# Kernel optimization log

Hardware: AMD Instinct MI355X
Metric: run time of the kernel (lower is better)

Reference implementation:

```python
import jax, jax.numpy as jnp
import numpy as np

B, O, L, E = 8, 4, 1024, 1024
BETA = 512
NSEG = 12
OUT = 1


def setup_inputs() -> dict:
    key = jax.random.key(0)
    ks = jax.random.split(key, 8)
    hidden = jax.random.normal(ks[0], (B, O, L, E), jnp.float32)
    # strictly increasing boundaries in (1, L), shared across the O options (as in the torch code)
    raw = jnp.sort(jax.random.randint(ks[1], (B, NSEG), 2, L - NSEG), axis=-1)
    idx = raw + jnp.arange(NSEG, dtype=raw.dtype)
    s = 0.02
    Wp = jax.random.normal(ks[2], (E, 2 * BETA), jnp.float32) * s
    bp = jnp.zeros((2 * BETA,), jnp.float32)
    Wa0 = jax.random.normal(ks[3], (2 * BETA, BETA), jnp.float32) * s
    ba0 = jnp.zeros((BETA,), jnp.float32)
    Wa = jax.random.normal(ks[4], (BETA, BETA), jnp.float32) * s
    ba = jnp.zeros((BETA,), jnp.float32)
    Wl0 = jax.random.normal(ks[5], (8 * BETA, BETA), jnp.float32) * s
    bl0 = jnp.zeros((BETA,), jnp.float32)
    Wl = jax.random.normal(ks[6], (BETA, OUT), jnp.float32) * s
    bl = jnp.zeros((OUT,), jnp.float32)
    return dict(hidden=hidden, idx=idx, Wp=Wp, bp=bp, Wa0=Wa0, ba0=ba0,
                Wa=Wa, ba=ba, Wl0=Wl0, bl0=bl0, Wl=Wl, bl=bl)


def _seg_mean(P, starts, ends):
    # P: [B,O,L+1,E] exclusive prefix sums; starts/ends: [B,K] token offsets.
    s = jnp.take_along_axis(P, starts[:, None, :, None], axis=2)
    e = jnp.take_along_axis(P, ends[:, None, :, None], axis=2)
    cnt = (ends - starts).astype(P.dtype)[:, None, :, None]
    return (e - s) / cnt  # [B,O,K,E]


def _get_param(x, Wp, bp):
    e = 1.0 + jax.nn.relu(x @ Wp + bp)
    a, b = jnp.split(e, 2, axis=-1)
    return a, b


def _attn_pool(a, b, Wa0, ba0, Wa, ba):
    # attention-weighted reduction over axis -2 (the 'logic' operator)
    h = jax.nn.relu(jnp.concatenate([a, b], axis=-1) @ Wa0 + ba0)
    w = jax.nn.softmax(h @ Wa + ba, axis=-2)
    return (w * a).sum(axis=-2), (w * b).sum(axis=-2)


def reference(hidden, idx, Wp, bp, Wa0, ba0, Wa, ba, Wl0, bl0, Wl, bl):
    # ---- init_embed: ragged segment means via prefix sums (one pass, no host syncs)
    P = jnp.concatenate([jnp.zeros_like(hidden[:, :, :1]),
                         jnp.cumsum(hidden, axis=2)], axis=2)  # [B,O,L+1,E]
    ones = jnp.ones((idx.shape[0], 1), idx.dtype)
    starts_c = jnp.concatenate([ones, idx[:, :NSEG - 3]], axis=1)  # [B, NSEG-2]
    ends_c = idx[:, :NSEG - 2]
    ctx = _seg_mean(P, starts_c, ends_c)                                # [B,O,Nc,E]
    q = _seg_mean(P, idx[:, NSEG - 3:NSEG - 2], idx[:, NSEG - 2:NSEG - 1])[:, :, 0]
    o = _seg_mean(P, idx[:, NSEG - 2:NSEG - 1], idx[:, NSEG - 1:NSEG])[:, :, 0]
    allc = _seg_mean(P, ones, idx[:, NSEG - 3:NSEG - 2])[:, :, 0]       # [B,O,E]
    # ---- beta params for context segments
    a_c, b_c = _get_param(ctx, Wp, bp)                                  # [B,O,Nc,BETA]
    # intersection over segments
    ia, ib = _attn_pool(a_c, b_c, Wa0, ba0, Wa, ba)                     # [B,O,BETA]
    # renew: pair each segment with the intersection, pool over the pair axis
    pa = jnp.stack([a_c, jnp.broadcast_to(ia[:, :, None, :], a_c.shape)], axis=-2)
    pb = jnp.stack([b_c, jnp.broadcast_to(ib[:, :, None, :], b_c.shape)], axis=-2)
    na, nb = _attn_pool(pa, pb, Wa0, ba0, Wa, ba)                       # [B,O,Nc,BETA]
    # union: invert, attention-pool over segments, invert back
    ua, ub = _attn_pool(1.0 / na, 1.0 / nb, Wa0, ba0, Wa, ba)
    ua, ub = 1.0 / ua, 1.0 / ub                                         # [B,O,BETA]
    # ---- beta params for question / option / whole-context spans
    a_q, b_q = _get_param(q, Wp, bp)
    a_o, b_o = _get_param(o, Wp, bp)
    a_ac, b_ac = _get_param(allc, Wp, bp)
    # ---- classify head: concat 4 beta embeddings -> 8*BETA -> MLP -> logits
    cat = jnp.concatenate([ua, ub, a_ac, b_ac, a_o, b_o, a_q, b_q], axis=-1)
    h = jax.nn.relu(cat @ Wl0 + bl0)
    return h @ Wl + bl  # [B,O,OUT]
```

## Files before the change

kernel.cpp:

```cpp
#include <hip/hip_runtime.h>
#include <hip/hip_bf16.h>

#define B_    8
#define O_    4
#define L_    1024
#define E_    1024
#define BETA_ 512
#define NSEG_ 12
#define BO_   32
#define NCH_  16

enum : size_t {
  WS_SPART = 0,
  WS_X     = WS_SPART + (size_t)BO_ * NCH_ * 12 * E_,
  WS_P1P   = WS_X     + (size_t)BO_ * 13 * E_,
  WS_H1P   = WS_P1P   + (size_t)8  * BO_ * 13 * E_,
  WS_T1P   = WS_H1P   + (size_t)16 * BO_ * 10 * BETA_,
  WS_H2P   = WS_T1P   + (size_t)8  * BO_ * 10 * BETA_,
  WS_T2P   = WS_H2P   + (size_t)8  * BO_ * BETA_,
  WS_H3P   = WS_T2P   + (size_t)8  * BO_ * BETA_,
  WS_T3P   = WS_H3P   + (size_t)16 * BO_ * 10 * BETA_,
  WS_HFP   = WS_T3P   + (size_t)8  * BO_ * 10 * BETA_,
  WS_TE    = WS_HFP   + (size_t)32 * BO_ * BETA_,
  WS_T1B   = WS_TE    + (size_t)BO_ * 13 * E_,
  WS_IAB   = WS_T1B   + (size_t)BO_ * 10 * BETA_,
  WS_RN    = WS_IAB   + (size_t)BO_ * 2 * BETA_,
  WS_END   = WS_RN    + (size_t)BO_ * 10 * E_,
};

__device__ __forceinline__ float relu_(float v) { return v > 0.f ? v : 0.f; }

__global__ void k1_segsum(const float* __restrict__ hidden, const int* __restrict__ idx,
                          float* __restrict__ Spart) {
    const int chunk = blockIdx.x;
    const int bo = blockIdx.y;
    const int b = bo >> 2;
    int cuts[13];
    cuts[0] = 1;
#pragma unroll
    for (int i = 0; i < 12; ++i) cuts[i + 1] = idx[b * NSEG_ + i];
    const int e4 = threadIdx.x << 2;
    float* sp = Spart + ((size_t)(bo * NCH_ + chunk) * 12) * E_ + e4;
    const float4 z = make_float4(0.f, 0.f, 0.f, 0.f);
#pragma unroll
    for (int m = 0; m < 12; ++m) *reinterpret_cast<float4*>(sp + (size_t)m * E_) = z;
    const int l0 = chunk * 64;
    const int l1 = l0 + 64;
    int lo = l0 < 1 ? 1 : l0;
    const int hi = l1 < cuts[12] ? l1 : cuts[12];
    if (lo >= hi) return;
    const float* base = hidden + (size_t)bo * (L_ * E_) + e4;
    int j = 0;
    while (j < 11 && cuts[j + 1] <= lo) ++j;
    int l = lo;
    while (l < hi) {
        const int e2 = (j < 11 && cuts[j + 1] < hi) ? cuts[j + 1] : hi;
        float sx = 0.f, sy = 0.f, sz = 0.f, sw = 0.f;
        for (; l < e2; ++l) {
            const float4 v = *reinterpret_cast<const float4*>(base + (size_t)l * E_);
            sx += v.x; sy += v.y; sz += v.z; sw += v.w;
        }
        float4 s; s.x = sx; s.y = sy; s.z = sz; s.w = sw;
        *reinterpret_cast<float4*>(sp + (size_t)j * E_) = s;
        ++j;
    }
}

__global__ __launch_bounds__(256) void k2_means(
    const float* __restrict__ Spart, const int* __restrict__ idx,
    float* __restrict__ X) {
    const int bo = blockIdx.y;
    const int col = blockIdx.x * 256 + threadIdx.x;
    const int b = bo >> 2;
    int cuts[13];
    cuts[0] = 1;
#pragma unroll
    for (int i = 0; i < 12; ++i) cuts[i + 1] = idx[b * NSEG_ + i];
    const float* sp = Spart + (size_t)bo * NCH_ * 12 * E_ + col;
    float allc = 0.f;
#pragma unroll
    for (int m = 0; m < 12; ++m) {
        float s = 0.f;
#pragma unroll
        for (int ch = 0; ch < NCH_; ++ch) s += sp[((size_t)ch * 12 + m) * E_];
        X[((size_t)bo * 13 + m) * E_ + col] = s / (float)(cuts[m + 1] - cuts[m]);
        if (m < 10) allc += s;
    }
    X[((size_t)bo * 13 + 12) * E_ + col] = allc / (float)(cuts[10] - 1);
}

template<int M, int ML, int K, int N, int KC, int BOG, int XF, int NPART>
__global__ __launch_bounds__(256) void gemm_sk(
    const float* __restrict__ Xb, const float* __restrict__ xbias,
    const float* __restrict__ W, float* __restrict__ OUT,
    const float* __restrict__ A0, const float* __restrict__ A1,
    const float* __restrict__ A2, const float* __restrict__ A3,
    float* __restrict__ SIDE, float* __restrict__ SIDE2) {
    const int kidx = blockIdx.x;
    const int k0 = kidx * KC;
    const int bo0 = blockIdx.y * BOG;
    const int c = blockIdx.z * 256 + threadIdx.x;
    const int tid = threadIdx.x;
    __shared__ __align__(16) float xs[BOG * ML * KC];

    for (int i = tid; i < BOG * ML * KC; i += 256) {
        const int kk = i % KC;
        const int rm = i / KC;
        const int m = rm % ML;
        const int bb = rm / ML;
        const int bo = bo0 + bb;
        const int k = k0 + kk;
        float v;
        if constexpr (XF == 0) {
            v = Xb[((size_t)bo * ML + m) * K + k];
        } else if constexpr (XF == 1) {
            float s = xbias[k];
#pragma unroll
            for (int p = 0; p < NPART; ++p)
                s += Xb[(((size_t)p * BO_ + bo) * ML + m) * K + k];
            v = 1.f + relu_(s);
            SIDE[((size_t)bo * ML + m) * K + k] = v;
        } else if constexpr (XF == 2) {
            float s = xbias[k];
#pragma unroll
            for (int p = 0; p < NPART; ++p)
                s += Xb[(((size_t)p * BO_ + bo) * ML + m) * K + k];
            v = relu_(s);
        } else if constexpr (XF == 4) {
            const int col = k & 511, half = k >> 9;
            const float bac = A2[col];
            float t[10], mx = -1e30f;
#pragma unroll
            for (int j = 0; j < 10; ++j) {
                float s = bac;
#pragma unroll
                for (int p = 0; p < NPART; ++p)
                    s += A0[(((size_t)p * BO_ + bo) * 10 + j) * BETA_ + col];
                t[j] = s;
                mx = fmaxf(mx, s);
            }
            if (half == 0) {
#pragma unroll
                for (int j = 0; j < 10; ++j)
                    SIDE2[((size_t)bo * 10 + j) * BETA_ + col] = t[j];
            }
            float sw = 0.f, acc = 0.f;
#pragma unroll
            for (int j = 0; j < 10; ++j) {
                const float pj = expf(t[j] - mx);
                sw += pj;
                acc = fmaf(pj, A1[((size_t)bo * 13 + j) * E_ + half * BETA_ + col], acc);
            }
            v = acc / sw;
            SIDE[(size_t)bo * 1024 + k] = v;
        } else if constexpr (XF == 5) {
            const int col = k & 511, half = k >> 9;
            const float tj = A0[((size_t)bo * 10 + m) * BETA_ + col];
            float tI = A2[col];
#pragma unroll
            for (int p = 0; p < NPART; ++p)
                tI += A1[((size_t)p * BO_ + bo) * BETA_ + col];
            const float mx = fmaxf(tj, tI);
            const float e0 = expf(tj - mx);
            const float e1 = expf(tI - mx);
            const float ea = A3[((size_t)bo * 13 + m) * E_ + half * BETA_ + col];
            const float iv = SIDE2[(size_t)bo * 1024 + k];
            v = (e0 + e1) / (e0 * ea + e1 * iv);
            SIDE[((size_t)bo * 10 + m) * E_ + k] = v;
        } else {
            if (k < 1024) {
                const int col = k & 511, half = k >> 9;
                const float bac = A2[col];
                float t[10], mx = -1e30f;
#pragma unroll
                for (int j = 0; j < 10; ++j) {
                    float s = bac;
#pragma unroll
                    for (int p = 0; p < NPART; ++p)
                        s += A0[(((size_t)p * BO_ + bo) * 10 + j) * BETA_ + col];
                    t[j] = s;
                    mx = fmaxf(mx, s);
                }
                float sw = 0.f, acc = 0.f;
#pragma unroll
                for (int j = 0; j < 10; ++j) {
                    const float pj = expf(t[j] - mx);
                    sw += pj;
                    acc = fmaf(pj, A1[((size_t)bo * 10 + j) * E_ + k], acc);
                }
                v = sw / acc;
            } else {
                const int region = k >> 10;
                const int row = (region == 1) ? 12 : (region == 2) ? 11 : 10;
                v = A3[((size_t)bo * 13 + row) * E_ + (k & 1023)];
            }
        }
        xs[i] = v;
    }
    __syncthreads();

    float acc[BOG][M];
#pragma unroll
    for (int b = 0; b < BOG; ++b)
#pragma unroll
        for (int m = 0; m < M; ++m) acc[b][m] = 0.f;
    const float* __restrict__ wp = W + (size_t)k0 * N + c;
    for (int k4 = 0; k4 < KC / 4; ++k4) {
        const float w0 = wp[(size_t)(4 * k4 + 0) * N];
        const float w1 = wp[(size_t)(4 * k4 + 1) * N];
        const float w2 = wp[(size_t)(4 * k4 + 2) * N];
        const float w3 = wp[(size_t)(4 * k4 + 3) * N];
#pragma unroll
        for (int b = 0; b < BOG; ++b) {
#pragma unroll
            for (int m = 0; m < M; ++m) {
                const float4 xv = *reinterpret_cast<const float4*>(&xs[(b * ML + m) * KC + 4 * k4]);
                float a = acc[b][m];
                a = fmaf(xv.x, w0, a);
                a = fmaf(xv.y, w1, a);
                a = fmaf(xv.z, w2, a);
                a = fmaf(xv.w, w3, a);
                acc[b][m] = a;
            }
        }
    }
#pragma unroll
    for (int b = 0; b < BOG; ++b) {
        float* op = OUT + (((size_t)kidx * BO_ + bo0 + b) * M) * N + c;
#pragma unroll
        for (int m = 0; m < M; ++m) op[(size_t)m * N] = acc[b][m];
    }
}

__global__ void __launch_bounds__(512) k_final(
    const float* __restrict__ HFP, const float* __restrict__ bl0,
    const float* __restrict__ Wl, const float* __restrict__ bl,
    float* __restrict__ out) {
    const int bo = blockIdx.x;
    const int c = threadIdx.x;
    float s = bl0[c];
#pragma unroll
    for (int p = 0; p < 32; ++p) s += HFP[((size_t)p * BO_ + bo) * BETA_ + c];
    float partial = relu_(s) * Wl[c];
#pragma unroll
    for (int off = 32; off > 0; off >>= 1) partial += __shfl_down(partial, off, 64);
    __shared__ float red[8];
    if ((c & 63) == 0) red[c >> 6] = partial;
    __syncthreads();
    if (c == 0) out[bo] = red[0] + red[1] + red[2] + red[3] + red[4] + red[5] + red[6] + red[7] + bl[0];
}

extern "C" void kernel_launch(void* const* d_in, const int* in_sizes, int n_in,
                              void* d_out, int out_size, void* d_ws, size_t ws_size,
                              hipStream_t stream) {
    const float* hidden = (const float*)d_in[0];
    const int* idx = (const int*)d_in[1];
    const float* Wp  = (const float*)d_in[2];
    const float* bp  = (const float*)d_in[3];
    const float* Wa0 = (const float*)d_in[4];
    const float* ba0 = (const float*)d_in[5];
    const float* Wa  = (const float*)d_in[6];
    const float* ba  = (const float*)d_in[7];
    const float* Wl0 = (const float*)d_in[8];
    const float* bl0 = (const float*)d_in[9];
    const float* Wl  = (const float*)d_in[10];
    const float* bl  = (const float*)d_in[11];
    float* ws = (float*)d_ws;
    float* SPART = ws + WS_SPART;
    float* X     = ws + WS_X;
    float* P1P   = ws + WS_P1P;
    float* H1P   = ws + WS_H1P;
    float* T1P   = ws + WS_T1P;
    float* H2P   = ws + WS_H2P;
    float* T2P   = ws + WS_T2P;
    float* H3P   = ws + WS_H3P;
    float* T3P   = ws + WS_T3P;
    float* HFP   = ws + WS_HFP;
    float* TE    = ws + WS_TE;
    float* T1B   = ws + WS_T1B;
    float* IAB   = ws + WS_IAB;
    float* RN    = ws + WS_RN;
    const float* NUL = nullptr;

    k1_segsum<<<dim3(NCH_, BO_), 256, 0, stream>>>(hidden, idx, SPART);
    k2_means<<<dim3(4, BO_), 256, 0, stream>>>(SPART, idx, X);
    gemm_sk<13, 13, 1024, 1024, 128, 2, 0, 1>
        <<<dim3(8, 16, 4), 256, 0, stream>>>(X, NUL, Wp, P1P, NUL, NUL, NUL, NUL, nullptr, nullptr);
    gemm_sk<10, 13, 1024, 512, 64, 2, 1, 8>
        <<<dim3(16, 16, 2), 256, 0, stream>>>(P1P, bp, Wa0, H1P, NUL, NUL, NUL, NUL, TE, nullptr);
    gemm_sk<10, 10, 512, 512, 64, 2, 2, 16>
        <<<dim3(8, 16, 2), 256, 0, stream>>>(H1P, ba0, Wa, T1P, NUL, NUL, NUL, NUL, nullptr, nullptr);
    gemm_sk<1, 1, 1024, 512, 128, 8, 4, 8>
        <<<dim3(8, 4, 2), 256, 0, stream>>>(NUL, NUL, Wa0, H2P, T1P, TE, ba, NUL, IAB, T1B);
    gemm_sk<1, 1, 512, 512, 64, 8, 2, 8>
        <<<dim3(8, 4, 2), 256, 0, stream>>>(H2P, ba0, Wa, T2P, NUL, NUL, NUL, NUL, nullptr, nullptr);
    gemm_sk<10, 10, 1024, 512, 64, 2, 5, 8>
        <<<dim3(16, 16, 2), 256, 0, stream>>>(NUL, NUL, Wa0, H3P, T1B, T2P, ba, TE, RN, IAB);
    gemm_sk<10, 10, 512, 512, 64, 2, 2, 16>
        <<<dim3(8, 16, 2), 256, 0, stream>>>(H3P, ba0, Wa, T3P, NUL, NUL, NUL, NUL, nullptr, nullptr);
    gemm_sk<1, 1, 4096, 512, 128, 8, 6, 8>
        <<<dim3(32, 4, 2), 256, 0, stream>>>(NUL, NUL, Wl0, HFP, T3P, RN, ba, TE, nullptr, nullptr);
    k_final<<<BO_, 512, 0, stream>>>(HFP, bl0, Wl, bl, (float*)d_out);
}
```

Before: 164.9 us.

## Unfuse GEMM prologues into separate reduction kernels and double segment-sum chunking

The split-K partial reductions, activations and softmax pooling that each GEMM used to compute in its shared-memory prologue move into small standalone kernels (t_te, t_hrelu, t_iab, t_rn, t_cat). The GEMM becomes a plain kernel that reads its input rows straight from global memory with float4 loads and has no shared staging. This removes the redundant prologue work repeated across every N-block, at the cost of more kernel launches and extra workspace round trips. The segment-sum pass also uses 32 chunks of 32 tokens instead of 16 of 64 and stops zero-filling partials; the means kernel now sums only the chunks that overlap each segment.

```diff
diff --git a/kernel.cpp b/kernel.cpp
--- a/kernel.cpp
+++ b/kernel.cpp
@@ -8,24 +8,28 @@
 #define BETA_ 512
 #define NSEG_ 12
 #define BO_   32
-#define NCH_  16
+#define NCH_  32
 
 enum : size_t {
   WS_SPART = 0,
   WS_X     = WS_SPART + (size_t)BO_ * NCH_ * 12 * E_,
   WS_P1P   = WS_X     + (size_t)BO_ * 13 * E_,
-  WS_H1P   = WS_P1P   + (size_t)8  * BO_ * 13 * E_,
-  WS_T1P   = WS_H1P   + (size_t)16 * BO_ * 10 * BETA_,
-  WS_H2P   = WS_T1P   + (size_t)8  * BO_ * 10 * BETA_,
-  WS_T2P   = WS_H2P   + (size_t)8  * BO_ * BETA_,
-  WS_H3P   = WS_T2P   + (size_t)8  * BO_ * BETA_,
-  WS_T3P   = WS_H3P   + (size_t)16 * BO_ * 10 * BETA_,
-  WS_HFP   = WS_T3P   + (size_t)8  * BO_ * 10 * BETA_,
-  WS_TE    = WS_HFP   + (size_t)32 * BO_ * BETA_,
-  WS_T1B   = WS_TE    + (size_t)BO_ * 13 * E_,
+  WS_TE    = WS_P1P   + (size_t)8  * BO_ * 13 * E_,
+  WS_H1P   = WS_TE    + (size_t)BO_ * 13 * E_,
+  WS_H1R   = WS_H1P   + (size_t)16 * BO_ * 10 * BETA_,
+  WS_T1P   = WS_H1R   + (size_t)BO_ * 10 * BETA_,
+  WS_T1B   = WS_T1P   + (size_t)8  * BO_ * 10 * BETA_,
   WS_IAB   = WS_T1B   + (size_t)BO_ * 10 * BETA_,
-  WS_RN    = WS_IAB   + (size_t)BO_ * 2 * BETA_,
-  WS_END   = WS_RN    + (size_t)BO_ * 10 * E_,
+  WS_H2P   = WS_IAB   + (size_t)BO_ * 2 * BETA_,
+  WS_H2R   = WS_H2P   + (size_t)8  * BO_ * BETA_,
+  WS_T2P   = WS_H2R   + (size_t)BO_ * BETA_,
+  WS_RN    = WS_T2P   + (size_t)8  * BO_ * BETA_,
+  WS_H3P   = WS_RN    + (size_t)BO_ * 10 * E_,
+  WS_H3R   = WS_H3P   + (size_t)16 * BO_ * 10 * BETA_,
+  WS_T3P   = WS_H3R   + (size_t)BO_ * 10 * BETA_,
+  WS_CAT   = WS_T3P   + (size_t)8  * BO_ * 10 * BETA_,
+  WS_HFP   = WS_CAT   + (size_t)BO_ * 8 * BETA_,
+  WS_END   = WS_HFP   + (size_t)32 * BO_ * BETA_,
 };
 
 __device__ __forceinline__ float relu_(float v) { return v > 0.f ? v : 0.f; }
@@ -39,17 +43,14 @@
     cuts[0] = 1;
 #pragma unroll
     for (int i = 0; i < 12; ++i) cuts[i + 1] = idx[b * NSEG_ + i];
-    const int e4 = threadIdx.x << 2;
-    float* sp = Spart + ((size_t)(bo * NCH_ + chunk) * 12) * E_ + e4;
-    const float4 z = make_float4(0.f, 0.f, 0.f, 0.f);
-#pragma unroll
-    for (int m = 0; m < 12; ++m) *reinterpret_cast<float4*>(sp + (size_t)m * E_) = z;
-    const int l0 = chunk * 64;
-    const int l1 = l0 + 64;
+    const int l0 = chunk * 32;
+    const int l1 = l0 + 32;
     int lo = l0 < 1 ? 1 : l0;
     const int hi = l1 < cuts[12] ? l1 : cuts[12];
     if (lo >= hi) return;
+    const int e4 = threadIdx.x << 2;
     const float* base = hidden + (size_t)bo * (L_ * E_) + e4;
+    float* sp = Spart + (size_t)(bo * NCH_ + chunk) * 12 * E_ + e4;
     int j = 0;
     while (j < 11 && cuts[j + 1] <= lo) ++j;
     int l = lo;
@@ -80,125 +81,24 @@
     float allc = 0.f;
 #pragma unroll
     for (int m = 0; m < 12; ++m) {
+        const int c0 = cuts[m] >> 5;
+        const int c1 = (cuts[m + 1] - 1) >> 5;
         float s = 0.f;
-#pragma unroll
-        for (int ch = 0; ch < NCH_; ++ch) s += sp[((size_t)ch * 12 + m) * E_];
+        for (int ch = c0; ch <= c1; ++ch) s += sp[((size_t)ch * 12 + m) * E_];
         X[((size_t)bo * 13 + m) * E_ + col] = s / (float)(cuts[m + 1] - cuts[m]);
         if (m < 10) allc += s;
     }
     X[((size_t)bo * 13 + 12) * E_ + col] = allc / (float)(cuts[10] - 1);
 }
 
-template<int M, int ML, int K, int N, int KC, int BOG, int XF, int NPART>
-__global__ __launch_bounds__(256) void gemm_sk(
-    const float* __restrict__ Xb, const float* __restrict__ xbias,
-    const float* __restrict__ W, float* __restrict__ OUT,
-    const float* __restrict__ A0, const float* __restrict__ A1,
-    const float* __restrict__ A2, const float* __restrict__ A3,
-    float* __restrict__ SIDE, float* __restrict__ SIDE2) {
+template<int M, int XM, int K, int N, int KC, int BOG>
+__global__ __launch_bounds__(256) void gemm_u(
+    const float* __restrict__ XR, const float* __restrict__ W,
+    float* __restrict__ OUTP) {
     const int kidx = blockIdx.x;
     const int k0 = kidx * KC;
     const int bo0 = blockIdx.y * BOG;
     const int c = blockIdx.z * 256 + threadIdx.x;
-    const int tid = threadIdx.x;
-    __shared__ __align__(16) float xs[BOG * ML * KC];
-
-    for (int i = tid; i < BOG * ML * KC; i += 256) {
-        const int kk = i % KC;
-        const int rm = i / KC;
-        const int m = rm % ML;
-        const int bb = rm / ML;
-        const int bo = bo0 + bb;
-        const int k = k0 + kk;
-        float v;
-        if constexpr (XF == 0) {
-            v = Xb[((size_t)bo * ML + m) * K + k];
-        } else if constexpr (XF == 1) {
-            float s = xbias[k];
-#pragma unroll
-            for (int p = 0; p < NPART; ++p)
-                s += Xb[(((size_t)p * BO_ + bo) * ML + m) * K + k];
-            v = 1.f + relu_(s);
-            SIDE[((size_t)bo * ML + m) * K + k] = v;
-        } else if constexpr (XF == 2) {
-            float s = xbias[k];
-#pragma unroll
-            for (int p = 0; p < NPART; ++p)
-                s += Xb[(((size_t)p * BO_ + bo) * ML + m) * K + k];
-            v = relu_(s);
-        } else if constexpr (XF == 4) {
-            const int col = k & 511, half = k >> 9;
-            const float bac = A2[col];
-            float t[10], mx = -1e30f;
-#pragma unroll
-            for (int j = 0; j < 10; ++j) {
-                float s = bac;
-#pragma unroll
-                for (int p = 0; p < NPART; ++p)
-                    s += A0[(((size_t)p * BO_ + bo) * 10 + j) * BETA_ + col];
-                t[j] = s;
-                mx = fmaxf(mx, s);
-            }
-            if (half == 0) {
-#pragma unroll
-                for (int j = 0; j < 10; ++j)
-                    SIDE2[((size_t)bo * 10 + j) * BETA_ + col] = t[j];
-            }
-            float sw = 0.f, acc = 0.f;
-#pragma unroll
-            for (int j = 0; j < 10; ++j) {
-                const float pj = expf(t[j] - mx);
-                sw += pj;
-                acc = fmaf(pj, A1[((size_t)bo * 13 + j) * E_ + half * BETA_ + col], acc);
-            }
-            v = acc / sw;
-            SIDE[(size_t)bo * 1024 + k] = v;
-        } else if constexpr (XF == 5) {
-            const int col = k & 511, half = k >> 9;
-            const float tj = A0[((size_t)bo * 10 + m) * BETA_ + col];
-            float tI = A2[col];
-#pragma unroll
-            for (int p = 0; p < NPART; ++p)
-                tI += A1[((size_t)p * BO_ + bo) * BETA_ + col];
-            const float mx = fmaxf(tj, tI);
-            const float e0 = expf(tj - mx);
-            const float e1 = expf(tI - mx);
-            const float ea = A3[((size_t)bo * 13 + m) * E_ + half * BETA_ + col];
-            const float iv = SIDE2[(size_t)bo * 1024 + k];
-            v = (e0 + e1) / (e0 * ea + e1 * iv);
-            SIDE[((size_t)bo * 10 + m) * E_ + k] = v;
-        } else {
-            if (k < 1024) {
-                const int col = k & 511, half = k >> 9;
-                const float bac = A2[col];
-                float t[10], mx = -1e30f;
-#pragma unroll
-                for (int j = 0; j < 10; ++j) {
-                    float s = bac;
-#pragma unroll
-                    for (int p = 0; p < NPART; ++p)
-                        s += A0[(((size_t)p * BO_ + bo) * 10 + j) * BETA_ + col];
-                    t[j] = s;
-                    mx = fmaxf(mx, s);
-                }
-                float sw = 0.f, acc = 0.f;
-#pragma unroll
-                for (int j = 0; j < 10; ++j) {
-                    const float pj = expf(t[j] - mx);
-                    sw += pj;
-                    acc = fmaf(pj, A1[((size_t)bo * 10 + j) * E_ + k], acc);
-                }
-                v = sw / acc;
-            } else {
-                const int region = k >> 10;
-                const int row = (region == 1) ? 12 : (region == 2) ? 11 : 10;
-                v = A3[((size_t)bo * 13 + row) * E_ + (k & 1023)];
-            }
-        }
-        xs[i] = v;
-    }
-    __syncthreads();
-
     float acc[BOG][M];
 #pragma unroll
     for (int b = 0; b < BOG; ++b)
@@ -214,7 +114,8 @@
         for (int b = 0; b < BOG; ++b) {
 #pragma unroll
             for (int m = 0; m < M; ++m) {
-                const float4 xv = *reinterpret_cast<const float4*>(&xs[(b * ML + m) * KC + 4 * k4]);
+                const float4 xv = *reinterpret_cast<const float4*>(
+                    XR + ((size_t)(bo0 + b) * XM + m) * K + k0 + 4 * k4);
                 float a = acc[b][m];
                 a = fmaf(xv.x, w0, a);
                 a = fmaf(xv.y, w1, a);
@@ -226,10 +127,120 @@
     }
 #pragma unroll
     for (int b = 0; b < BOG; ++b) {
-        float* op = OUT + (((size_t)kidx * BO_ + bo0 + b) * M) * N + c;
+        float* op = OUTP + (((size_t)kidx * BO_ + bo0 + b) * M) * N + c;
 #pragma unroll
         for (int m = 0; m < M; ++m) op[(size_t)m * N] = acc[b][m];
     }
+}
+
+__global__ __launch_bounds__(256) void t_te(
+    const float* __restrict__ P1P, const float* __restrict__ bp,
+    float* __restrict__ TE, float* __restrict__ CAT) {
+    const int bo = blockIdx.y;
+    const int i = blockIdx.x * 256 + threadIdx.x;
+    const int m = i >> 10, col = i & 1023;
+    float s = bp[col];
+#pragma unroll
+    for (int p = 0; p < 8; ++p)
+        s += P1P[(((size_t)p * BO_ + bo) * 13 + m) * E_ + col];
+    const float v = 1.f + relu_(s);
+    TE[((size_t)bo * 13 + m) * E_ + col] = v;
+    if (m >= 10) CAT[(size_t)bo * 4096 + (size_t)(13 - m) * 1024 + col] = v;
+}
+
+template<int NPART, int ROWS>
+__global__ __launch_bounds__(256) void t_hrelu(
+    const float* __restrict__ HP, const float* __restrict__ b,
+    float* __restrict__ HR) {
+    const int bo = blockIdx.y;
+    const int i = blockIdx.x * 256 + threadIdx.x;
+    const int col = i & 511;
+    float s = b[col];
+#pragma unroll
+    for (int p = 0; p < NPART; ++p)
+        s += HP[((size_t)p * BO_ + bo) * (ROWS * BETA_) + i];
+    HR[(size_t)bo * (ROWS * BETA_) + i] = relu_(s);
+}
+
+__global__ void __launch_bounds__(512) t_iab(
+    const float* __restrict__ T1P, const float* __restrict__ ba,
+    const float* __restrict__ TE, float* __restrict__ T1B,
+    float* __restrict__ IAB) {
+    const int bo = blockIdx.x;
+    const int c = threadIdx.x;
+    const float bac = ba[c];
+    float t[10], mx = -1e30f;
+#pragma unroll
+    for (int j = 0; j < 10; ++j) {
+        float s = bac;
+#pragma unroll
+        for (int p = 0; p < 8; ++p)
+            s += T1P[(((size_t)p * BO_ + bo) * 10 + j) * BETA_ + c];
+        t[j] = s;
+        T1B[((size_t)bo * 10 + j) * BETA_ + c] = s;
+        mx = fmaxf(mx, s);
+    }
+    float p[10], sw = 0.f;
+#pragma unroll
+    for (int j = 0; j < 10; ++j) { p[j] = expf(t[j] - mx); sw += p[j]; }
+    const float inv = 1.0f / sw;
+    float ia = 0.f, ib = 0.f;
+#pragma unroll
+    for (int j = 0; j < 10; ++j) {
+        const float pj = p[j] * inv;
+        ia = fmaf(pj, TE[((size_t)bo * 13 + j) * E_ + c], ia);
+        ib = fmaf(pj, TE[((size_t)bo * 13 + j) * E_ + BETA_ + c], ib);
+    }
+    IAB[(size_t)bo * 1024 + c] = ia;
+    IAB[(size_t)bo * 1024 + BETA_ + c] = ib;
+}
+
+__global__ __launch_bounds__(256) void t_rn(
+    const float* __restrict__ T1B, const float* __restrict__ T2P,
+    const float* __restrict__ ba, const float* __restrict__ TE,
+    const float* __restrict__ IAB, float* __restrict__ RN) {
+    const int bo = blockIdx.y;
+    const int i = blockIdx.x * 256 + threadIdx.x;
+    const int j = i >> 10, k = i & 1023;
+    const int col = k & 511;
+    const float tj = T1B[((size_t)bo * 10 + j) * BETA_ + col];
+    float tI = ba[col];
+#pragma unroll
+    for (int p = 0; p < 8; ++p)
+        tI += T2P[((size_t)p * BO_ + bo) * BETA_ + col];
+    const float mx = fmaxf(tj, tI);
+    const float e0 = expf(tj - mx);
+    const float e1 = expf(tI - mx);
+    const float ea = TE[((size_t)bo * 13 + j) * E_ + k];
+    const float iv = IAB[(size_t)bo * 1024 + k];
+    RN[((size_t)bo * 10 + j) * E_ + k] = (e0 + e1) / (e0 * ea + e1 * iv);
+}
+
+__global__ __launch_bounds__(256) void t_cat(
+    const float* __restrict__ T3P, const float* __restrict__ ba,
+    const float* __restrict__ RN, float* __restrict__ CAT) {
+    const int bo = blockIdx.y;
+    const int k = blockIdx.x * 256 + threadIdx.x;
+    const int col = k & 511;
+    const float bac = ba[col];
+    float t[10], mx = -1e30f;
+#pragma unroll
+    for (int j = 0; j < 10; ++j) {
+        float s = bac;
+#pragma unroll
+        for (int p = 0; p < 8; ++p)
+            s += T3P[(((size_t)p * BO_ + bo) * 10 + j) * BETA_ + col];
+        t[j] = s;
+        mx = fmaxf(mx, s);
+    }
+    float sw = 0.f, acc = 0.f;
+#pragma unroll
+    for (int j = 0; j < 10; ++j) {
+        const float pj = expf(t[j] - mx);
+        sw += pj;
+        acc = fmaf(pj, RN[((size_t)bo * 10 + j) * E_ + k], acc);
+    }
+    CAT[(size_t)bo * 4096 + k] = sw / acc;
 }
 
 __global__ void __launch_bounds__(512) k_final(
@@ -269,36 +280,46 @@
     float* SPART = ws + WS_SPART;
     float* X     = ws + WS_X;
     float* P1P   = ws + WS_P1P;
+    float* TE    = ws + WS_TE;
     float* H1P   = ws + WS_H1P;
+    float* H1R   = ws + WS_H1R;
     float* T1P   = ws + WS_T1P;
-    float* H2P   = ws + WS_H2P;
-    float* T2P   = ws + WS_T2P;
-    float* H3P   = ws + WS_H3P;
-    float* T3P   = ws + WS_T3P;
-    float* HFP   = ws + WS_HFP;
-    float* TE    = ws + WS_TE;
     float* T1B   = ws + WS_T1B;
     float* IAB   = ws + WS_IAB;
+    float* H2P   = ws + WS_H2P;
+    float* H2R   = ws + WS_H2R;
+    float* T2P   = ws + WS_T2P;
     float* RN    = ws + WS_RN;
-    const float* NUL = nullptr;
+    float* H3P   = ws + WS_H3P;
+    float* H3R   = ws + WS_H3R;
+    float* T3P   = ws + WS_T3P;
+    float* CAT   = ws + WS_CAT;
+    float* HFP   = ws + WS_HFP;
 
     k1_segsum<<<dim3(NCH_, BO_), 256, 0, stream>>>(hidden, idx, SPART);
     k2_means<<<dim3(4, BO_), 256, 0, stream>>>(SPART, idx, X);
-    gemm_sk<13, 13, 1024, 1024, 128, 2, 0, 1>
-        <<<dim3(8, 16, 4), 256, 0, stream>>>(X, NUL, Wp, P1P, NUL, NUL, NUL, NUL, nullptr, nullptr);
-    gemm_sk<10, 13, 1024, 512, 64, 2, 1, 8>
-        <<<dim3(16, 16, 2), 256, 0, stream>>>(P1P, bp, Wa0, H1P, NUL, NUL, NUL, NUL, TE, nullptr);
-    gemm_sk<10, 10, 512, 512, 64, 2, 2, 16>
-        <<<dim3(8, 16, 2), 256, 0, stream>>>(H1P, ba0, Wa, T1P, NUL, NUL, NUL, NUL, nullptr, nullptr);
-    gemm_sk<1, 1, 1024, 512, 128, 8, 4, 8>
-        <<<dim3(8, 4, 2), 256, 0, stream>>>(NUL, NUL, Wa0, H2P, T1P, TE, ba, NUL, IAB, T1B);
-    gemm_sk<1, 1, 512, 512, 64, 8, 2, 8>
-        <<<dim3(8, 4, 2), 256, 0, stream>>>(H2P, ba0, Wa, T2P, NUL, NUL, NUL, NUL, nullptr, nullptr);
-    gemm_sk<10, 10, 1024, 512, 64, 2, 5, 8>
-        <<<dim3(16, 16, 2), 256, 0, stream>>>(NUL, NUL, Wa0, H3P, T1B, T2P, ba, TE, RN, IAB);
-    gemm_sk<10, 10, 512, 512, 64, 2, 2, 16>
-        <<<dim3(8, 16, 2), 256, 0, stream>>>(H3P, ba0, Wa, T3P, NUL, NUL, NUL, NUL, nullptr, nullptr);
-    gemm_sk<1, 1, 4096, 512, 128, 8, 6, 8>
-        <<<dim3(32, 4, 2), 256, 0, stream>>>(NUL, NUL, Wl0, HFP, T3P, RN, ba, TE, nullptr, nullptr);
+    gemm_u<13, 13, 1024, 1024, 128, 2>
+        <<<dim3(8, 16, 4), 256, 0, stream>>>(X, Wp, P1P);
+    t_te<<<dim3(52, BO_), 256, 0, stream>>>(P1P, bp, TE, CAT);
+    gemm_u<10, 13, 1024, 512, 64, 2>
+        <<<dim3(16, 16, 2), 256, 0, stream>>>(TE, Wa0, H1P);
+    t_hrelu<16, 10><<<dim3(20, BO_), 256, 0, stream>>>(H1P, ba0, H1R);
+    gemm_u<10, 10, 512, 512, 64, 2>
+        <<<dim3(8, 16, 2), 256, 0, stream>>>(H1R, Wa, T1P);
+    t_iab<<<BO_, 512, 0, stream>>>(T1P, ba, TE, T1B, IAB);
+    gemm_u<1, 1, 1024, 512, 128, 2>
+        <<<dim3(8, 16, 2), 256, 0, stream>>>(IAB, Wa0, H2P);
+    t_hrelu<8, 1><<<dim3(2, BO_), 256, 0, stream>>>(H2P, ba0, H2R);
+    gemm_u<1, 1, 512, 512, 64, 2>
+        <<<dim3(8, 16, 2), 256, 0, stream>>>(H2R, Wa, T2P);
+    t_rn<<<dim3(40, BO_), 256, 0, stream>>>(T1B, T2P, ba, TE, IAB, RN);
+    gemm_u<10, 10, 1024, 512, 64, 2>
+        <<<dim3(16, 16, 2), 256, 0, stream>>>(RN, Wa0, H3P);
+    t_hrelu<16, 10><<<dim3(20, BO_), 256, 0, stream>>>(H3P, ba0, H3R);
+    gemm_u<10, 10, 512, 512, 64, 2>
+        <<<dim3(8, 16, 2), 256, 0, stream>>>(H3R, Wa, T3P);
+    t_cat<<<dim3(4, BO_), 256, 0, stream>>>(T3P, ba, RN, CAT);
+    gemm_u<1, 1, 4096, 512, 128, 8>
+        <<<dim3(32, 4, 2), 256, 0, stream>>>(CAT, Wl0, HFP);
     k_final<<<BO_, 512, 0, stream>>>(HFP, bl0, Wl, bl, (float*)d_out);
 }
```

Result: slower. 170.8 us (+3.6%).

## Fuse all stages into one cooperative persistent kernel with grid barriers

Applied to the files above, without the earlier changes.

Replaces the eleven separate kernel launches with a single cooperatively launched persistent kernel of 512 blocks. The stages are separated by atomic-counter grid barriers, and each stage loops over its tasks inside the kernel. The segment-sum chunks are halved to 32 rows, and the means stage now reads only the chunks that overlap each segment instead of all of them. Unused chunk partials are no longer zero-filled. The intent is to remove launch and inter-kernel gaps. In exchange it relies on all blocks being co-resident, and spinning barriers cost time on phases that have few tasks.

```diff
diff --git a/kernel.cpp b/kernel.cpp
--- a/kernel.cpp
+++ b/kernel.cpp
@@ -8,167 +8,85 @@
 #define BETA_ 512
 #define NSEG_ 12
 #define BO_   32
-#define NCH_  16
+#define NCH_  32
+#define NBLK  512
 
 enum : size_t {
-  WS_SPART = 0,
+  WS_BAR   = 0,
+  WS_SPART = 64,
   WS_X     = WS_SPART + (size_t)BO_ * NCH_ * 12 * E_,
   WS_P1P   = WS_X     + (size_t)BO_ * 13 * E_,
-  WS_H1P   = WS_P1P   + (size_t)8  * BO_ * 13 * E_,
+  WS_TE    = WS_P1P   + (size_t)8  * BO_ * 13 * E_,
+  WS_H1P   = WS_TE    + (size_t)BO_ * 13 * E_,
   WS_T1P   = WS_H1P   + (size_t)16 * BO_ * 10 * BETA_,
-  WS_H2P   = WS_T1P   + (size_t)8  * BO_ * 10 * BETA_,
+  WS_T1B   = WS_T1P   + (size_t)8  * BO_ * 10 * BETA_,
+  WS_IAB   = WS_T1B   + (size_t)BO_ * 10 * BETA_,
+  WS_H2P   = WS_IAB   + (size_t)BO_ * 2 * BETA_,
   WS_T2P   = WS_H2P   + (size_t)8  * BO_ * BETA_,
-  WS_H3P   = WS_T2P   + (size_t)8  * BO_ * BETA_,
+  WS_RN    = WS_T2P   + (size_t)8  * BO_ * BETA_,
+  WS_H3P   = WS_RN    + (size_t)BO_ * 10 * E_,
   WS_T3P   = WS_H3P   + (size_t)16 * BO_ * 10 * BETA_,
   WS_HFP   = WS_T3P   + (size_t)8  * BO_ * 10 * BETA_,
-  WS_TE    = WS_HFP   + (size_t)32 * BO_ * BETA_,
-  WS_T1B   = WS_TE    + (size_t)BO_ * 13 * E_,
-  WS_IAB   = WS_T1B   + (size_t)BO_ * 10 * BETA_,
-  WS_RN    = WS_IAB   + (size_t)BO_ * 2 * BETA_,
-  WS_END   = WS_RN    + (size_t)BO_ * 10 * E_,
+  WS_END   = WS_HFP   + (size_t)32 * BO_ * BETA_,
 };
 
 __device__ __forceinline__ float relu_(float v) { return v > 0.f ? v : 0.f; }
 
-__global__ void k1_segsum(const float* __restrict__ hidden, const int* __restrict__ idx,
-                          float* __restrict__ Spart) {
-    const int chunk = blockIdx.x;
-    const int bo = blockIdx.y;
-    const int b = bo >> 2;
-    int cuts[13];
-    cuts[0] = 1;
-#pragma unroll
-    for (int i = 0; i < 12; ++i) cuts[i + 1] = idx[b * NSEG_ + i];
-    const int e4 = threadIdx.x << 2;
-    float* sp = Spart + ((size_t)(bo * NCH_ + chunk) * 12) * E_ + e4;
-    const float4 z = make_float4(0.f, 0.f, 0.f, 0.f);
-#pragma unroll
-    for (int m = 0; m < 12; ++m) *reinterpret_cast<float4*>(sp + (size_t)m * E_) = z;
-    const int l0 = chunk * 64;
-    const int l1 = l0 + 64;
-    int lo = l0 < 1 ? 1 : l0;
-    const int hi = l1 < cuts[12] ? l1 : cuts[12];
-    if (lo >= hi) return;
-    const float* base = hidden + (size_t)bo * (L_ * E_) + e4;
-    int j = 0;
-    while (j < 11 && cuts[j + 1] <= lo) ++j;
-    int l = lo;
-    while (l < hi) {
-        const int e2 = (j < 11 && cuts[j + 1] < hi) ? cuts[j + 1] : hi;
-        float sx = 0.f, sy = 0.f, sz = 0.f, sw = 0.f;
-        for (; l < e2; ++l) {
-            const float4 v = *reinterpret_cast<const float4*>(base + (size_t)l * E_);
-            sx += v.x; sy += v.y; sz += v.z; sw += v.w;
-        }
-        float4 s; s.x = sx; s.y = sy; s.z = sz; s.w = sw;
-        *reinterpret_cast<float4*>(sp + (size_t)j * E_) = s;
-        ++j;
-    }
+__device__ __forceinline__ void gbar(unsigned* bar, unsigned tgt, int tid) {
+    __syncthreads();
+    if (tid == 0) {
+        __threadfence();
+        __hip_atomic_fetch_add(bar, 1u, __ATOMIC_RELAXED, __HIP_MEMORY_SCOPE_AGENT);
+        while (__hip_atomic_load(bar, __ATOMIC_RELAXED, __HIP_MEMORY_SCOPE_AGENT) < tgt)
+            __builtin_amdgcn_s_sleep(16);
+        __threadfence();
+    }
+    __syncthreads();
 }
 
-__global__ __launch_bounds__(256) void k2_means(
-    const float* __restrict__ Spart, const int* __restrict__ idx,
-    float* __restrict__ X) {
-    const int bo = blockIdx.y;
-    const int col = blockIdx.x * 256 + threadIdx.x;
-    const int b = bo >> 2;
-    int cuts[13];
-    cuts[0] = 1;
-#pragma unroll
-    for (int i = 0; i < 12; ++i) cuts[i + 1] = idx[b * NSEG_ + i];
-    const float* sp = Spart + (size_t)bo * NCH_ * 12 * E_ + col;
-    float allc = 0.f;
-#pragma unroll
-    for (int m = 0; m < 12; ++m) {
-        float s = 0.f;
-#pragma unroll
-        for (int ch = 0; ch < NCH_; ++ch) s += sp[((size_t)ch * 12 + m) * E_];
-        X[((size_t)bo * 13 + m) * E_ + col] = s / (float)(cuts[m + 1] - cuts[m]);
-        if (m < 10) allc += s;
-    }
-    X[((size_t)bo * 13 + 12) * E_ + col] = allc / (float)(cuts[10] - 1);
-}
-
 template<int M, int ML, int K, int N, int KC, int BOG, int XF, int NPART>
-__global__ __launch_bounds__(256) void gemm_sk(
+__device__ void gemm_phase(
+    const int gid, const int tid, const int NT, float* xs,
     const float* __restrict__ Xb, const float* __restrict__ xbias,
     const float* __restrict__ W, float* __restrict__ OUT,
     const float* __restrict__ A0, const float* __restrict__ A1,
     const float* __restrict__ A2, const float* __restrict__ A3,
     float* __restrict__ SIDE, float* __restrict__ SIDE2) {
-    const int kidx = blockIdx.x;
-    const int k0 = kidx * KC;
-    const int bo0 = blockIdx.y * BOG;
-    const int c = blockIdx.z * 256 + threadIdx.x;
-    const int tid = threadIdx.x;
-    __shared__ __align__(16) float xs[BOG * ML * KC];
-
-    for (int i = tid; i < BOG * ML * KC; i += 256) {
-        const int kk = i % KC;
-        const int rm = i / KC;
-        const int m = rm % ML;
-        const int bb = rm / ML;
-        const int bo = bo0 + bb;
-        const int k = k0 + kk;
-        float v;
-        if constexpr (XF == 0) {
-            v = Xb[((size_t)bo * ML + m) * K + k];
-        } else if constexpr (XF == 1) {
-            float s = xbias[k];
-#pragma unroll
-            for (int p = 0; p < NPART; ++p)
-                s += Xb[(((size_t)p * BO_ + bo) * ML + m) * K + k];
-            v = 1.f + relu_(s);
-            SIDE[((size_t)bo * ML + m) * K + k] = v;
-        } else if constexpr (XF == 2) {
-            float s = xbias[k];
-#pragma unroll
-            for (int p = 0; p < NPART; ++p)
-                s += Xb[(((size_t)p * BO_ + bo) * ML + m) * K + k];
-            v = relu_(s);
-        } else if constexpr (XF == 4) {
-            const int col = k & 511, half = k >> 9;
-            const float bac = A2[col];
-            float t[10], mx = -1e30f;
-#pragma unroll
-            for (int j = 0; j < 10; ++j) {
-                float s = bac;
+    constexpr int NCH = N / 256;
+    constexpr int NBOG = BO_ / BOG;
+    for (int task = gid; task < NT; task += NBLK) {
+        const int nidx = task % NCH;
+        const int rest = task / NCH;
+        const int bidx = rest % NBOG;
+        const int kidx = rest / NBOG;
+        const int k0 = kidx * KC;
+        const int bo0 = bidx * BOG;
+        const int c = nidx * 256 + tid;
+
+        for (int i = tid; i < BOG * ML * KC; i += 256) {
+            const int kk = i % KC;
+            const int rm = i / KC;
+            const int m = rm % ML;
+            const int bb = rm / ML;
+            const int bo = bo0 + bb;
+            const int k = k0 + kk;
+            float v;
+            if constexpr (XF == 0) {
+                v = Xb[((size_t)bo * ML + m) * K + k];
+            } else if constexpr (XF == 1) {
+                float s = xbias[k];
 #pragma unroll
                 for (int p = 0; p < NPART; ++p)
-                    s += A0[(((size_t)p * BO_ + bo) * 10 + j) * BETA_ + col];
-                t[j] = s;
-                mx = fmaxf(mx, s);
-            }
-            if (half == 0) {
-#pragma unroll
-                for (int j = 0; j < 10; ++j)
-                    SIDE2[((size_t)bo * 10 + j) * BETA_ + col] = t[j];
-            }
-            float sw = 0.f, acc = 0.f;
-#pragma unroll
-            for (int j = 0; j < 10; ++j) {
-                const float pj = expf(t[j] - mx);
-                sw += pj;
-                acc = fmaf(pj, A1[((size_t)bo * 13 + j) * E_ + half * BETA_ + col], acc);
-            }
-            v = acc / sw;
-            SIDE[(size_t)bo * 1024 + k] = v;
-        } else if constexpr (XF == 5) {
-            const int col = k & 511, half = k >> 9;
-            const float tj = A0[((size_t)bo * 10 + m) * BETA_ + col];
-            float tI = A2[col];
-#pragma unroll
-            for (int p = 0; p < NPART; ++p)
-                tI += A1[((size_t)p * BO_ + bo) * BETA_ + col];
-            const float mx = fmaxf(tj, tI);
-            const float e0 = expf(tj - mx);
-            const float e1 = expf(tI - mx);
-            const float ea = A3[((size_t)bo * 13 + m) * E_ + half * BETA_ + col];
-            const float iv = SIDE2[(size_t)bo * 1024 + k];
-            v = (e0 + e1) / (e0 * ea + e1 * iv);
-            SIDE[((size_t)bo * 10 + m) * E_ + k] = v;
-        } else {
-            if (k < 1024) {
+                    s += Xb[(((size_t)p * BO_ + bo) * ML + m) * K + k];
+                v = 1.f + relu_(s);
+                SIDE[((size_t)bo * ML + m) * K + k] = v;
+            } else if constexpr (XF == 2) {
+                float s = xbias[k];
+#pragma unroll
+                for (int p = 0; p < NPART; ++p)
+                    s += Xb[(((size_t)p * BO_ + bo) * ML + m) * K + k];
+                v = relu_(s);
+            } else if constexpr (XF == 4) {
                 const int col = k & 511, half = k >> 9;
                 const float bac = A2[col];
                 float t[10], mx = -1e30f;
@@ -181,73 +99,230 @@
                     t[j] = s;
                     mx = fmaxf(mx, s);
                 }
+                if (half == 0) {
+#pragma unroll
+                    for (int j = 0; j < 10; ++j)
+                        SIDE2[((size_t)bo * 10 + j) * BETA_ + col] = t[j];
+                }
                 float sw = 0.f, acc = 0.f;
 #pragma unroll
                 for (int j = 0; j < 10; ++j) {
                     const float pj = expf(t[j] - mx);
                     sw += pj;
-                    acc = fmaf(pj, A1[((size_t)bo * 10 + j) * E_ + k], acc);
-                }
-                v = sw / acc;
+                    acc = fmaf(pj, A1[((size_t)bo * 13 + j) * E_ + half * BETA_ + col], acc);
+                }
+                v = acc / sw;
+                SIDE[(size_t)bo * 1024 + k] = v;
+            } else if constexpr (XF == 5) {
+                const int col = k & 511, half = k >> 9;
+                const float tj = A0[((size_t)bo * 10 + m) * BETA_ + col];
+                float tI = A2[col];
+#pragma unroll
+                for (int p = 0; p < NPART; ++p)
+                    tI += A1[((size_t)p * BO_ + bo) * BETA_ + col];
+                const float mx = fmaxf(tj, tI);
+                const float e0 = expf(tj - mx);
+                const float e1 = expf(tI - mx);
+                const float ea = A3[((size_t)bo * 13 + m) * E_ + half * BETA_ + col];
+                const float iv = SIDE2[(size_t)bo * 1024 + k];
+                v = (e0 + e1) / (e0 * ea + e1 * iv);
+                SIDE[((size_t)bo * 10 + m) * E_ + k] = v;
             } else {
-                const int region = k >> 10;
-                const int row = (region == 1) ? 12 : (region == 2) ? 11 : 10;
-                v = A3[((size_t)bo * 13 + row) * E_ + (k & 1023)];
+                if (k < 1024) {
+                    const int col = k & 511;
+                    const float bac = A2[col];
+                    float t[10], mx = -1e30f;
+#pragma unroll
+                    for (int j = 0; j < 10; ++j) {
+                        float s = bac;
+#pragma unroll
+                        for (int p = 0; p < NPART; ++p)
+                            s += A0[(((size_t)p * BO_ + bo) * 10 + j) * BETA_ + col];
+                        t[j] = s;
+                        mx = fmaxf(mx, s);
+                    }
+                    float sw = 0.f, acc = 0.f;
+#pragma unroll
+                    for (int j = 0; j < 10; ++j) {
+                        const float pj = expf(t[j] - mx);
+                        sw += pj;
+                        acc = fmaf(pj, A1[((size_t)bo * 10 + j) * E_ + k], acc);
+                    }
+                    v = sw / acc;
+                } else {
+                    const int region = k >> 10;
+                    const int row = (region == 1) ? 12 : (region == 2) ? 11 : 10;
+                    v = A3[((size_t)bo * 13 + row) * E_ + (k & 1023)];
+                }
             }
-        }
-        xs[i] = v;
-    }
-    __syncthreads();
-
-    float acc[BOG][M];
-#pragma unroll
-    for (int b = 0; b < BOG; ++b)
-#pragma unroll
-        for (int m = 0; m < M; ++m) acc[b][m] = 0.f;
-    const float* __restrict__ wp = W + (size_t)k0 * N + c;
-    for (int k4 = 0; k4 < KC / 4; ++k4) {
-        const float w0 = wp[(size_t)(4 * k4 + 0) * N];
-        const float w1 = wp[(size_t)(4 * k4 + 1) * N];
-        const float w2 = wp[(size_t)(4 * k4 + 2) * N];
-        const float w3 = wp[(size_t)(4 * k4 + 3) * N];
+            xs[i] = v;
+        }
+        __syncthreads();
+
+        float acc[BOG][M];
+#pragma unroll
+        for (int b = 0; b < BOG; ++b)
+#pragma unroll
+            for (int m = 0; m < M; ++m) acc[b][m] = 0.f;
+        const float* __restrict__ wp = W + (size_t)k0 * N + c;
+        for (int k4 = 0; k4 < KC / 4; ++k4) {
+            const float w0 = wp[(size_t)(4 * k4 + 0) * N];
+            const float w1 = wp[(size_t)(4 * k4 + 1) * N];
+            const float w2 = wp[(size_t)(4 * k4 + 2) * N];
+            const float w3 = wp[(size_t)(4 * k4 + 3) * N];
+#pragma unroll
+            for (int b = 0; b < BOG; ++b) {
+#pragma unroll
+                for (int m = 0; m < M; ++m) {
+                    const float4 xv = *reinterpret_cast<const float4*>(&xs[(b * ML + m) * KC + 4 * k4]);
+                    float a = acc[b][m];
+                    a = fmaf(xv.x, w0, a);
+                    a = fmaf(xv.y, w1, a);
+                    a = fmaf(xv.z, w2, a);
+                    a = fmaf(xv.w, w3, a);
+                    acc[b][m] = a;
+                }
+            }
+        }
 #pragma unroll
         for (int b = 0; b < BOG; ++b) {
-#pragma unroll
-            for (int m = 0; m < M; ++m) {
-                const float4 xv = *reinterpret_cast<const float4*>(&xs[(b * ML + m) * KC + 4 * k4]);
-                float a = acc[b][m];
-                a = fmaf(xv.x, w0, a);
-                a = fmaf(xv.y, w1, a);
-                a = fmaf(xv.z, w2, a);
-                a = fmaf(xv.w, w3, a);
-                acc[b][m] = a;
+            float* op = OUT + (((size_t)kidx * BO_ + bo0 + b) * M) * N + c;
+#pragma unroll
+            for (int m = 0; m < M; ++m) op[(size_t)m * N] = acc[b][m];
+        }
+        __syncthreads();
+    }
+}
+
+__global__ void __launch_bounds__(256, 2) pipeline(
+    const float* __restrict__ hidden, const int* __restrict__ idx,
+    const float* __restrict__ Wp, const float* __restrict__ bp,
+    const float* __restrict__ Wa0, const float* __restrict__ ba0,
+    const float* __restrict__ Wa, const float* __restrict__ ba,
+    const float* __restrict__ Wl0, const float* __restrict__ bl0,
+    const float* __restrict__ Wl, const float* __restrict__ bl,
+    float* __restrict__ ws, float* __restrict__ out) {
+    const int gid = blockIdx.x;
+    const int tid = threadIdx.x;
+    __shared__ __align__(16) float xs[2 * 13 * 128];
+
+    unsigned* bar = reinterpret_cast<unsigned*>(ws + WS_BAR);
+    float* SPART = ws + WS_SPART;
+    float* X     = ws + WS_X;
+    float* P1P   = ws + WS_P1P;
+    float* TE    = ws + WS_TE;
+    float* H1P   = ws + WS_H1P;
+    float* T1P   = ws + WS_T1P;
+    float* T1B   = ws + WS_T1B;
+    float* IAB   = ws + WS_IAB;
+    float* H2P   = ws + WS_H2P;
+    float* T2P   = ws + WS_T2P;
+    float* RN    = ws + WS_RN;
+    float* H3P   = ws + WS_H3P;
+    float* T3P   = ws + WS_T3P;
+    float* HFP   = ws + WS_HFP;
+    const float* NUL = nullptr;
+
+    for (int task = gid; task < NCH_ * BO_; task += NBLK) {
+        const int chunk = task & (NCH_ - 1);
+        const int bo = task >> 5;
+        const int b = bo >> 2;
+        int cuts[13];
+        cuts[0] = 1;
+#pragma unroll
+        for (int i = 0; i < 12; ++i) cuts[i + 1] = idx[b * NSEG_ + i];
+        const int l0 = chunk * 32;
+        const int l1 = l0 + 32;
+        int lo = l0 < 1 ? 1 : l0;
+        const int hi = l1 < cuts[12] ? l1 : cuts[12];
+        if (lo >= hi) continue;
+        const int e4 = tid << 2;
+        const float* base = hidden + (size_t)bo * (L_ * E_) + e4;
+        float* sp = SPART + (size_t)(bo * NCH_ + chunk) * 12 * E_ + e4;
+        int j = 0;
+        while (j < 11 && cuts[j + 1] <= lo) ++j;
+        int l = lo;
+        while (l < hi) {
+            const int e2 = (j < 11 && cuts[j + 1] < hi) ? cuts[j + 1] : hi;
+            float sx = 0.f, sy = 0.f, sz = 0.f, sw = 0.f;
+            for (; l < e2; ++l) {
+                const float4 v = *reinterpret_cast<const float4*>(base + (size_t)l * E_);
+                sx += v.x; sy += v.y; sz += v.z; sw += v.w;
             }
-        }
-    }
-#pragma unroll
-    for (int b = 0; b < BOG; ++b) {
-        float* op = OUT + (((size_t)kidx * BO_ + bo0 + b) * M) * N + c;
-#pragma unroll
-        for (int m = 0; m < M; ++m) op[(size_t)m * N] = acc[b][m];
-    }
-}
-
-__global__ void __launch_bounds__(512) k_final(
-    const float* __restrict__ HFP, const float* __restrict__ bl0,
-    const float* __restrict__ Wl, const float* __restrict__ bl,
-    float* __restrict__ out) {
-    const int bo = blockIdx.x;
-    const int c = threadIdx.x;
-    float s = bl0[c];
-#pragma unroll
-    for (int p = 0; p < 32; ++p) s += HFP[((size_t)p * BO_ + bo) * BETA_ + c];
-    float partial = relu_(s) * Wl[c];
-#pragma unroll
-    for (int off = 32; off > 0; off >>= 1) partial += __shfl_down(partial, off, 64);
-    __shared__ float red[8];
-    if ((c & 63) == 0) red[c >> 6] = partial;
-    __syncthreads();
-    if (c == 0) out[bo] = red[0] + red[1] + red[2] + red[3] + red[4] + red[5] + red[6] + red[7] + bl[0];
+            float4 s; s.x = sx; s.y = sy; s.z = sz; s.w = sw;
+            *reinterpret_cast<float4*>(sp + (size_t)j * E_) = s;
+            ++j;
+        }
+    }
+    gbar(bar, NBLK * 1, tid);
+
+    for (int task = gid; task < 128; task += NBLK) {
+        const int bo = task >> 2;
+        const int col = (task & 3) * 256 + tid;
+        const int b = bo >> 2;
+        int cuts[13];
+        cuts[0] = 1;
+#pragma unroll
+        for (int i = 0; i < 12; ++i) cuts[i + 1] = idx[b * NSEG_ + i];
+        const float* sp = SPART + (size_t)bo * NCH_ * 12 * E_ + col;
+        float allc = 0.f;
+#pragma unroll
+        for (int m = 0; m < 12; ++m) {
+            const int c0 = cuts[m] >> 5;
+            const int c1 = (cuts[m + 1] - 1) >> 5;
+            float s = 0.f;
+            for (int ch = c0; ch <= c1; ++ch) s += sp[((size_t)ch * 12 + m) * E_];
+            X[((size_t)bo * 13 + m) * E_ + col] = s / (float)(cuts[m + 1] - cuts[m]);
+            if (m < 10) allc += s;
+        }
+        X[((size_t)bo * 13 + 12) * E_ + col] = allc / (float)(cuts[10] - 1);
+    }
+    gbar(bar, NBLK * 2, tid);
+
+    gemm_phase<13, 13, 1024, 1024, 128, 2, 0, 1>(gid, tid, 512, xs, X, NUL, Wp, P1P,
+                                                 NUL, NUL, NUL, NUL, nullptr, nullptr);
+    gbar(bar, NBLK * 3, tid);
+    gemm_phase<10, 13, 1024, 512, 64, 2, 1, 8>(gid, tid, 512, xs, P1P, bp, Wa0, H1P,
+                                               NUL, NUL, NUL, NUL, TE, nullptr);
+    gbar(bar, NBLK * 4, tid);
+    gemm_phase<10, 10, 512, 512, 64, 2, 2, 16>(gid, tid, 256, xs, H1P, ba0, Wa, T1P,
+                                               NUL, NUL, NUL, NUL, nullptr, nullptr);
+    gbar(bar, NBLK * 5, tid);
+    gemm_phase<1, 1, 1024, 512, 128, 8, 4, 8>(gid, tid, 64, xs, NUL, NUL, Wa0, H2P,
+                                              T1P, TE, ba, NUL, IAB, T1B);
+    gbar(bar, NBLK * 6, tid);
+    gemm_phase<1, 1, 512, 512, 64, 8, 2, 8>(gid, tid, 64, xs, H2P, ba0, Wa, T2P,
+                                            NUL, NUL, NUL, NUL, nullptr, nullptr);
+    gbar(bar, NBLK * 7, tid);
+    gemm_phase<10, 10, 1024, 512, 64, 2, 5, 8>(gid, tid, 512, xs, NUL, NUL, Wa0, H3P,
+                                               T1B, T2P, ba, TE, RN, IAB);
+    gbar(bar, NBLK * 8, tid);
+    gemm_phase<10, 10, 512, 512, 64, 2, 2, 16>(gid, tid, 256, xs, H3P, ba0, Wa, T3P,
+                                               NUL, NUL, NUL, NUL, nullptr, nullptr);
+    gbar(bar, NBLK * 9, tid);
+    gemm_phase<1, 1, 4096, 512, 128, 8, 6, 8>(gid, tid, 256, xs, NUL, NUL, Wl0, HFP,
+                                              T3P, RN, ba, TE, nullptr, nullptr);
+    gbar(bar, NBLK * 10, tid);
+
+    for (int task = gid; task < BO_; task += NBLK) {
+        const int bo = task;
+        float partial = 0.f;
+#pragma unroll
+        for (int h = 0; h < 2; ++h) {
+            const int c = h * 256 + tid;
+            float s = bl0[c];
+#pragma unroll
+            for (int p = 0; p < 32; ++p) s += HFP[((size_t)p * BO_ + bo) * BETA_ + c];
+            partial = fmaf(relu_(s), Wl[c], partial);
+        }
+#pragma unroll
+        for (int off = 32; off > 0; off >>= 1) partial += __shfl_down(partial, off, 64);
+        __syncthreads();
+        if ((tid & 63) == 0) xs[tid >> 6] = partial;
+        __syncthreads();
+        if (tid == 0) out[bo] = xs[0] + xs[1] + xs[2] + xs[3] + bl[0];
+        __syncthreads();
+    }
 }
 
 extern "C" void kernel_launch(void* const* d_in, const int* in_sizes, int n_in,
@@ -266,39 +341,14 @@
     const float* Wl  = (const float*)d_in[10];
     const float* bl  = (const float*)d_in[11];
     float* ws = (float*)d_ws;
-    float* SPART = ws + WS_SPART;
-    float* X     = ws + WS_X;
-    float* P1P   = ws + WS_P1P;
-    float* H1P   = ws + WS_H1P;
-    float* T1P   = ws + WS_T1P;
-    float* H2P   = ws + WS_H2P;
-    float* T2P   = ws + WS_T2P;
-    float* H3P   = ws + WS_H3P;
-    float* T3P   = ws + WS_T3P;
-    float* HFP   = ws + WS_HFP;
-    float* TE    = ws + WS_TE;
-    float* T1B   = ws + WS_T1B;
-    float* IAB   = ws + WS_IAB;
-    float* RN    = ws + WS_RN;
-    const float* NUL = nullptr;
-
-    k1_segsum<<<dim3(NCH_, BO_), 256, 0, stream>>>(hidden, idx, SPART);
-    k2_means<<<dim3(4, BO_), 256, 0, stream>>>(SPART, idx, X);
-    gemm_sk<13, 13, 1024, 1024, 128, 2, 0, 1>
-        <<<dim3(8, 16, 4), 256, 0, stream>>>(X, NUL, Wp, P1P, NUL, NUL, NUL, NUL, nullptr, nullptr);
-    gemm_sk<10, 13, 1024, 512, 64, 2, 1, 8>
-        <<<dim3(16, 16, 2), 256, 0, stream>>>(P1P, bp, Wa0, H1P, NUL, NUL, NUL, NUL, TE, nullptr);
-    gemm_sk<10, 10, 512, 512, 64, 2, 2, 16>
-        <<<dim3(8, 16, 2), 256, 0, stream>>>(H1P, ba0, Wa, T1P, NUL, NUL, NUL, NUL, nullptr, nullptr);
-    gemm_sk<1, 1, 1024, 512, 128, 8, 4, 8>
-        <<<dim3(8, 4, 2), 256, 0, stream>>>(NUL, NUL, Wa0, H2P, T1P, TE, ba, NUL, IAB, T1B);
-    gemm_sk<1, 1, 512, 512, 64, 8, 2, 8>
-        <<<dim3(8, 4, 2), 256, 0, stream>>>(H2P, ba0, Wa, T2P, NUL, NUL, NUL, NUL, nullptr, nullptr);
-    gemm_sk<10, 10, 1024, 512, 64, 2, 5, 8>
-        <<<dim3(16, 16, 2), 256, 0, stream>>>(NUL, NUL, Wa0, H3P, T1B, T2P, ba, TE, RN, IAB);
-    gemm_sk<10, 10, 512, 512, 64, 2, 2, 16>
-        <<<dim3(8, 16, 2), 256, 0, stream>>>(H3P, ba0, Wa, T3P, NUL, NUL, NUL, NUL, nullptr, nullptr);
-    gemm_sk<1, 1, 4096, 512, 128, 8, 6, 8>
-        <<<dim3(32, 4, 2), 256, 0, stream>>>(NUL, NUL, Wl0, HFP, T3P, RN, ba, TE, nullptr, nullptr);
-    k_final<<<BO_, 512, 0, stream>>>(HFP, bl0, Wl, bl, (float*)d_out);
+    float* out = (float*)d_out;
+
+    hipMemsetAsync(d_ws, 0, 256, stream);
+    void* kargs[] = {
+        (void*)&hidden, (void*)&idx, (void*)&Wp, (void*)&bp,
+        (void*)&Wa0, (void*)&ba0, (void*)&Wa, (void*)&ba,
+        (void*)&Wl0, (void*)&bl0, (void*)&Wl, (void*)&bl,
+        (void*)&ws, (void*)&out,
+    };
+    hipLaunchCooperativeKernel((const void*)pipeline, dim3(NBLK), dim3(256), kargs, 0, stream);
 }
```

Result: slower. 646.2 us (+292.0%).
